# Kernel optimization log

Hardware: AMD Instinct MI355X
Metric: run time of the kernel (lower is better)

Reference implementation:

```python
import jax, jax.numpy as jnp
import numpy as np

LAM = 1e-05
NUM_POINTS = 300
THRESHOLD = 0.5


def _sobel(img):
    # img: [B, 1, H, W] -> edge magnitude [B, 1, H, W]
    kx = jnp.array([[-1., 0., 1.], [-2., 0., 2.], [-1., 0., 1.]], jnp.float32).reshape(1, 1, 3, 3)
    ky = jnp.array([[-1., -2., -1.], [0., 0., 0.], [1., 2., 1.]], jnp.float32).reshape(1, 1, 3, 3)
    dn = jax.lax.conv_dimension_numbers(img.shape, kx.shape, ('NCHW', 'OIHW', 'NCHW'))
    ex = jax.lax.conv_general_dilated(img, kx, (1, 1), ((1, 1), (1, 1)), dimension_numbers=dn)
    ey = jax.lax.conv_general_dilated(img, ky, (1, 1), ((1, 1), (1, 1)), dimension_numbers=dn)
    return jnp.sqrt(ex ** 2 + ey ** 2)


def _select_points(edge_map, key):
    # JIT-friendly analogue of nonzero + randperm[:300]: random scores on
    # above-threshold pixels, take top NUM_POINTS; invalid slots are padded
    # with a duplicate of the first valid point (zero-length MST edges, so
    # they contribute nothing to total persistence, matching fewer points).
    H, W = edge_map.shape
    flat = edge_map.reshape(-1)
    mask = flat > THRESHOLD
    scores = jnp.where(mask, jax.random.uniform(key, flat.shape), -jnp.inf)
    _, idx = jax.lax.top_k(scores, NUM_POINTS)
    valid = mask[idx]
    pts = jnp.stack([idx // W, idx % W], axis=-1).astype(jnp.float32)  # (row, col)
    pts = jnp.where(valid[:, None], pts, pts[0])
    return pts


def _mst_total_persistence(pts):
    # H0 persistence of a Vietoris-Rips complex: births are 0, deaths are the
    # MST edge lengths (Prim's algorithm via lax.scan over N-1 steps).
    # total_persistence with exponent q=2: sum(death^2).
    d2 = jnp.sum((pts[:, None, :] - pts[None, :, :]) ** 2, axis=-1)
    D = jnp.sqrt(jnp.maximum(d2, 0.0))  # [N, N]
    n = pts.shape[0]
    in_tree = jnp.zeros((n,), dtype=bool).at[0].set(True)

    def step(carry, _):
        in_tree, mind = carry
        m = jnp.where(in_tree, jnp.inf, mind)
        j = jnp.argmin(m)
        w = m[j]
        in_tree = in_tree.at[j].set(True)
        mind = jnp.minimum(mind, D[j])
        return (in_tree, mind), w

    _, deaths = jax.lax.scan(step, (in_tree, D[0]), None, length=n - 1)
    return jnp.sum(deaths ** 2)


def _topo_loss(model_output, labels):
    pred_edges = _sobel(jax.nn.sigmoid(model_output))[:, 0]  # [B, H, W]
    mask_edges = _sobel(labels)[:, 0]                         # [B, H, W]
    B = pred_edges.shape[0]
    keys = jax.random.split(jax.random.key(42), 2 * B).reshape(B, 2)

    def per_sample(pe, me, k):
        pts_p = _select_points(pe, k[0])
        pts_m = _select_points(me, k[1])
        tp_p = _mst_total_persistence(pts_p)
        tp_m = _mst_total_persistence(pts_m)
        # SummaryStatisticLoss(total_persistence): |stat(mask) - stat(pred)|
        return jnp.abs(tp_m - tp_p)

    losses = jax.vmap(per_sample)(pred_edges, mask_edges, keys)
    return LAM * jnp.sum(losses) / B


def setup_inputs() -> dict:
    key = jax.random.key(0)
    k1, k2 = jax.random.split(key)
    model_output = jax.random.normal(k1, (32, 1, 512, 512), dtype=jnp.float32)
    labels = jax.random.uniform(k2, (32, 1, 512, 512), dtype=jnp.float32)
    return {"model_output": model_output, "labels": labels}


def reference(model_output, labels):
    return _topo_loss(model_output, labels)
```

## Files before the change

### kernel.cpp

```cpp
#include <hip/hip_runtime.h>
#include <cstdint>
#include <cstddef>

#define NPIX (512 * 512)
#define NMAPS 64
#define NPTS 300
#define CAP 1024
#define LCAP 640
#define NWORDS 4096
#define TARGET 700.0
#define MT_FIXED 8368608u

__device__ __forceinline__ uint32_t umin32(uint32_t a, uint32_t b) {
  return a < b ? a : b;
}

__device__ __forceinline__ void tf2x32(uint32_t k0, uint32_t k1,
                                       uint32_t x0, uint32_t x1,
                                       uint32_t& o0, uint32_t& o1) {
  uint32_t ks2 = k0 ^ k1 ^ 0x1BD11BDAu;
#define TFR(r) { x0 += x1; x1 = (x1 << (r)) | (x1 >> (32 - (r))); x1 ^= x0; }
  x0 += k0; x1 += k1;
  TFR(13) TFR(15) TFR(26) TFR(6)
  x0 += k1; x1 += ks2 + 1u;
  TFR(17) TFR(29) TFR(16) TFR(24)
  x0 += ks2; x1 += k0 + 2u;
  TFR(13) TFR(15) TFR(26) TFR(6)
  x0 += k0; x1 += k1 + 3u;
  TFR(17) TFR(29) TFR(16) TFR(24)
  x0 += k1; x1 += ks2 + 4u;
  TFR(13) TFR(15) TFR(26) TFR(6)
  x0 += ks2; x1 += k0 + 5u;
#undef TFR
  o0 = x0; o1 = x1;
}

__device__ __forceinline__ uint32_t score23(uint32_t k0, uint32_t k1, uint32_t p) {
  uint32_t a, b;
  tf2x32(k0, k1, 0u, p, a, b);
  return (a ^ b) >> 9;
}

__device__ __forceinline__ void map_key(int m, uint32_t& k0, uint32_t& k1) {
  tf2x32(0u, 42u, 0u, (uint32_t)m, k0, k1);
}

template <int CTRL>
__device__ __forceinline__ uint32_t dpp_mov_u32(uint32_t x) {
  return (uint32_t)__builtin_amdgcn_update_dpp((int)x, (int)x, CTRL, 0xF, 0xF,
                                               false);
}

__device__ __forceinline__ uint32_t wave_min_u32_bcast(uint32_t v) {
  v = umin32(v, dpp_mov_u32<0x111>(v));
  v = umin32(v, dpp_mov_u32<0x112>(v));
  v = umin32(v, dpp_mov_u32<0x114>(v));
  v = umin32(v, dpp_mov_u32<0x118>(v));
  v = umin32(v, dpp_mov_u32<0x142>(v));
  v = umin32(v, dpp_mov_u32<0x143>(v));
  return (uint32_t)__builtin_amdgcn_readlane((int)v, 63);
}

__global__ __launch_bounds__(256) void edge_collect_kernel(
    const float* __restrict__ mo, const float* __restrict__ lb,
    unsigned long long* __restrict__ bitmap, unsigned int* __restrict__ wcnts,
    unsigned long long* __restrict__ cand, unsigned int* __restrict__ gcnt32,
    float* __restrict__ out) {
  const int m = blockIdx.y;
  const int which = m & 1;
  const float* __restrict__ src = (which ? lb : mo) + (size_t)(m >> 1) * NPIX;
  const int l = threadIdx.x & 63;
  const int wi = blockIdx.x * 4 + (threadIdx.x >> 6);
  const int cs = wi & 7;
  const int seg = wi >> 3;
  const int y0 = seg * 32;
  const int X = cs * 64 + l;
  const int hcol = (l == 0) ? X - 1 : ((l == 63) ? X + 1 : -1);

  if (m == 0 && blockIdx.x == 0 && threadIdx.x == 0) out[0] = 0.f;

  __shared__ unsigned long long lbuf[LCAP];
  __shared__ unsigned int lcnt;
  __shared__ unsigned int lbase;
  if (threadIdx.x == 0) lcnt = 0;
  __syncthreads();

  uint32_t k0, k1;
  map_key(m, k0, k1);

  auto sig = [&](float t) {
    return which ? t : 1.f / (1.f + __expf(-t));
  };
  auto ldmain = [&](int row) -> float {
    return ((unsigned)row < 512u) ? sig(src[row * 512 + X]) : 0.f;
  };
  auto ldhalo = [&](int row) -> float {
    return ((unsigned)row < 512u && (unsigned)hcol < 512u)
               ? sig(src[row * 512 + hcol]) : 0.f;
  };

  float a = ldmain(y0 - 1), ha = ldhalo(y0 - 1);
  float b = ldmain(y0),     hb = ldhalo(y0);
  unsigned int cnt = 0;

  for (int i = 0; i < 32; ++i) {
    const int y = y0 + i;
    float c = ldmain(y + 1), hc = ldhalo(y + 1);

    float aL = __shfl_up(a, 1);   if (l == 0)  aL = ha;
    float aR = __shfl_down(a, 1); if (l == 63) aR = ha;
    float bL = __shfl_up(b, 1);   if (l == 0)  bL = hb;
    float bR = __shfl_down(b, 1); if (l == 63) bR = hb;
    float cL = __shfl_up(c, 1);   if (l == 0)  cL = hc;
    float cR = __shfl_down(c, 1); if (l == 63) cR = hc;

    float ex = (aR - aL) + 2.f * (bR - bL) + (cR - cL);
    float ey = (cL + 2.f * c + cR) - (aL + 2.f * a + aR);
    bool bit = (ex * ex + ey * ey) > 0.25f;

    unsigned long long ball = __ballot(bit);
    if (l == 0) {
      bitmap[(size_t)m * NWORDS + (size_t)y * 8 + cs] = ball;
      cnt += (unsigned int)__popcll(ball);
    }
    if (bit) {
      uint32_t p = (uint32_t)(y * 512 + X);
      uint32_t sc = score23(k0, k1, p);
      if (sc >= MT_FIXED) {
        unsigned int pos = atomicAdd(&lcnt, 1u);
        if (pos < LCAP)
          lbuf[pos] = ((unsigned long long)sc << 32) | (uint32_t)(~p);
      }
    }
    a = b; ha = hb; b = c; hb = hc;
  }
  if (l == 0) wcnts[m * 128 + wi] = cnt;

  __syncthreads();
  unsigned int cc = lcnt < LCAP ? lcnt : LCAP;
  if (threadIdx.x == 0)
    lbase = atomicAdd(&gcnt32[m * 32], lcnt + (lcnt > LCAP ? 0x1000000u : 0u));
  __syncthreads();
  for (unsigned int i = threadIdx.x; i < cc; i += 256) {
    unsigned int pos = lbase + i;
    if (pos < CAP) cand[(size_t)m * CAP + pos] = lbuf[i];
  }
}

__device__ __forceinline__ void reduce_N(const unsigned int* __restrict__ wcnts,
                                         int m, int tid, unsigned int* sN) {
  if (tid < 64) {
    unsigned int v = wcnts[m * 128 + tid] + wcnts[m * 128 + 64 + tid];
#pragma unroll
    for (int off = 32; off > 0; off >>= 1) v += __shfl_xor(v, off, 64);
    if (tid == 0) *sN = v;
  }
}

__global__ __launch_bounds__(256) void select_kernel(
    const unsigned long long* __restrict__ bitmap,
    const unsigned int* __restrict__ wcnts,
    const unsigned long long* __restrict__ cand,
    const unsigned int* __restrict__ gcnt32,
    uint32_t* __restrict__ pts, unsigned int* __restrict__ nsel) {
  const int m = blockIdx.x;
  const int tid = threadIdx.x;
  __shared__ unsigned long long buf[CAP];
  __shared__ unsigned int hist[256];
  __shared__ unsigned int s_tot, s_cnt, s_b, s_rank, sN;

  reduce_N(wcnts, m, tid, &sN);
  __syncthreads();
  const unsigned int N = sN;
  if (N == 0) { if (tid == 0) nsel[m] = 0; return; }
  const unsigned int need = N < NPTS ? N : NPTS;

  unsigned int c;
  const unsigned int g = gcnt32[m * 32];
  if (g >= need && g <= CAP) {
    c = g;
    for (unsigned int i = tid; i < c; i += 256)
      buf[i] = cand[(size_t)m * CAP + i];
    __syncthreads();
  } else {
    uint32_t k0, k1;
    map_key(m, k0, k1);
    const unsigned long long* __restrict__ wmap = bitmap + (size_t)m * NWORDS;
    unsigned int mt = 0, cnt = 0;
    double target = TARGET;
    for (int iter = 0; iter < 16; ++iter) {
      mt = ((double)N > target)
               ? (unsigned int)(8388608.0 * (1.0 - target / (double)N))
               : 0u;
      if (tid == 0) s_tot = 0;
      __syncthreads();
      unsigned int lc = 0;
      for (int w = tid; w < NWORDS; w += 256) {
        unsigned long long word = wmap[w];
        while (word) {
          int bpos = __builtin_ctzll(word);
          word &= word - 1;
          uint32_t p = ((uint32_t)w << 6) + (uint32_t)bpos;
          lc += (score23(k0, k1, p) >= mt) ? 1u : 0u;
        }
      }
      if (lc) atomicAdd(&s_tot, lc);
      __syncthreads();
      cnt = s_tot;
      __syncthreads();
      if (cnt >= need && cnt <= CAP) break;
      if (cnt < need) target *= 3.0; else target *= 0.5;
    }
    if (tid == 0) s_cnt = 0;
    __syncthreads();
    for (int w = tid; w < NWORDS; w += 256) {
      unsigned long long word = wmap[w];
      while (word) {
        int bpos = __builtin_ctzll(word);
        word &= word - 1;
        uint32_t p = ((uint32_t)w << 6) + (uint32_t)bpos;
        uint32_t sc = score23(k0, k1, p);
        if (sc >= mt) {
          unsigned int pos = atomicAdd(&s_cnt, 1u);
          if (pos < CAP)
            buf[pos] = ((unsigned long long)sc << 32) | (uint32_t)(~p);
        }
      }
    }
    __syncthreads();
    c = s_cnt < CAP ? s_cnt : CAP;
    __syncthreads();
  }

  unsigned long long T = 0ull;
  if (c > need) {
    unsigned int rank = need;
    unsigned long long prefix = 0ull;
    for (int sh = 48; sh >= 0; sh -= 8) {
      hist[tid] = 0;
      __syncthreads();
      for (unsigned int i = tid; i < c; i += 256) {
        unsigned long long k = buf[i];
        if ((k >> (sh + 8)) == (prefix >> (sh + 8)))
          atomicAdd(&hist[(unsigned int)(k >> sh) & 255u], 1u);
      }
      __syncthreads();
      if (tid < 64) {
        unsigned int h0 = hist[4 * tid], h1 = hist[4 * tid + 1];
        unsigned int h2 = hist[4 * tid + 2], h3 = hist[4 * tid + 3];
        unsigned int gsum = h0 + h1 + h2 + h3;
        unsigned int s = gsum;
#pragma unroll
        for (int off = 1; off < 64; off <<= 1) {
          unsigned int o = __shfl_down(s, off, 64);
          s += (tid + off < 64) ? o : 0u;
        }
        unsigned int above = s - gsum;
        unsigned int S3 = above, S2 = S3 + h3, S1 = S2 + h2, S0 = S1 + h1;
        if (S3 < rank && rank <= S3 + h3) { s_b = 4 * tid + 3; s_rank = rank - S3; }
        if (S2 < rank && rank <= S2 + h2) { s_b = 4 * tid + 2; s_rank = rank - S2; }
        if (S1 < rank && rank <= S1 + h1) { s_b = 4 * tid + 1; s_rank = rank - S1; }
        if (S0 < rank && rank <= S0 + h0) { s_b = 4 * tid + 0; s_rank = rank - S0; }
      }
      __syncthreads();
      prefix |= ((unsigned long long)s_b) << sh;
      rank = s_rank;
    }
    T = prefix;
  }

  if (tid == 0) s_cnt = 0;
  __syncthreads();
  for (unsigned int i = tid; i < c; i += 256) {
    unsigned long long k = buf[i];
    if (k >= T) {
      unsigned int pos = atomicAdd(&s_cnt, 1u);
      if (pos < NPTS) {
        uint32_t p = ~(uint32_t)k;
        pts[(size_t)m * NPTS + pos] = ((p >> 9) << 16) | (p & 511u);
      }
    }
  }
  __syncthreads();
  if (tid == 0) nsel[m] = s_cnt < need ? s_cnt : need;
}

__global__ __launch_bounds__(128, 1) void mst_kernel(
    const uint32_t* __restrict__ pts, const unsigned int* __restrict__ nsel,
    float* __restrict__ out) {
  const int wv = threadIdx.x >> 6;
  const int m = blockIdx.x * 2 + wv;
  const int l = threadIdx.x & 63;
  const int n = (int)nsel[m];
  __shared__ float stp[2];

  unsigned int utp = 0;
  if (n > 1) {
    uint32_t pk[5], key[5];
    int px[5], py[5];
#pragma unroll
    for (int k = 0; k < 5; ++k) {
      int id = k * 64 + l;
      pk[k] = (id < n) ? pts[(size_t)m * NPTS + id] : 0u;
    }
    const uint32_t p0 = (uint32_t)__builtin_amdgcn_readlane((int)pk[0], 0);
    const int x0 = (int)(p0 >> 16), y0 = (int)(p0 & 0xFFFFu);
#pragma unroll
    for (int k = 0; k < 5; ++k) {
      int id = k * 64 + l;
      px[k] = (int)(pk[k] >> 16);
      py[k] = (int)(pk[k] & 0xFFFFu);
      if (id > 0 && id < n) {
        int dx = px[k] - x0, dy = py[k] - y0;
        key[k] = ((uint32_t)(__mul24(dx, dx) + __mul24(dy, dy)) << 9) |
                 (uint32_t)id;
      } else {
        key[k] = 0xFFFFFFFFu;
      }
    }

    for (int it = 0; it < n - 1; ++it) {
      uint32_t best = umin32(umin32(umin32(key[0], key[1]),
                                    umin32(key[2], key[3])), key[4]);
      best = wave_min_u32_bcast(best);
      utp += best >> 9;
      const int j = (int)(best & 511u);
      const int ko = j >> 6, lo = j & 63;
      uint32_t cp = pk[0];
#pragma unroll
      for (int k = 1; k < 5; ++k) cp = (ko == k) ? pk[k] : cp;
      const uint32_t pj = (uint32_t)__builtin_amdgcn_readlane((int)cp, lo);
      const int jx = (int)(pj >> 16), jy = (int)(pj & 0xFFFFu);
#pragma unroll
      for (int k = 0; k < 5; ++k) {
        int dx = px[k] - jx, dy = py[k] - jy;
        uint32_t nk = ((uint32_t)(__mul24(dx, dx) + __mul24(dy, dy)) << 9) |
                      (uint32_t)(k * 64 + l);
        uint32_t upd =
            (key[k] == 0xFFFFFFFFu) ? 0xFFFFFFFFu : umin32(key[k], nk);
        key[k] = (k == ko && l == lo) ? 0xFFFFFFFFu : upd;
      }
    }
  }
  if (l == 0) stp[wv] = (float)utp;
  __syncthreads();
  if (threadIdx.x == 0)
    atomicAdd(out, 1e-5f * fabsf(stp[1] - stp[0]) / 32.f);
}

extern "C" void kernel_launch(void* const* d_in, const int* in_sizes, int n_in,
                              void* d_out, int out_size, void* d_ws,
                              size_t ws_size, hipStream_t stream) {
  const float* mo = (const float*)d_in[0];
  const float* lb = (const float*)d_in[1];
  float* out = (float*)d_out;
  char* ws = (char*)d_ws;

  unsigned long long* bitmap = (unsigned long long*)ws;
  unsigned long long* cand = (unsigned long long*)(ws + 2097152);
  unsigned int* wcnts  = (unsigned int*)(ws + 2621440);
  unsigned int* gcnt32 = (unsigned int*)(ws + 2654208);
  unsigned int* nsel   = (unsigned int*)(ws + 2662400);
  uint32_t* pts        = (uint32_t*)(ws + 2662656);

  hipMemsetAsync(gcnt32, 0, 8192, stream);
  edge_collect_kernel<<<dim3(32, 64), 256, 0, stream>>>(mo, lb, bitmap, wcnts,
                                                        cand, gcnt32, out);
  select_kernel<<<NMAPS, 256, 0, stream>>>(bitmap, wcnts, cand, gcnt32, pts,
                                           nsel);
  mst_kernel<<<32, 128, 0, stream>>>(pts, nsel, out);
}
```

Baseline: 246.8 us.

## Use per-block candidate slots, separable Sobel, and templated bounds checks in edge pass

Candidate collection now gives each block a fixed slot region and its own count, so the global atomic counter and its memset launch are gone. The select kernel compacts these regions using a prefix sum over the block counts. The Sobel stencil is computed separably, which cuts the shuffles per row from six to four. Edge-body variants are templated on sigmoid-versus-identity and on whether the tile touches the image border, so interior tiles skip row bounds checks. The raw threefry bits are compared against a threshold instead of calling score23, and the larger CAP grows the select kernel's shared buffer to 16KB.

```diff
diff --git a/kernel.cpp b/kernel.cpp
--- a/kernel.cpp
+++ b/kernel.cpp
@@ -5,11 +5,12 @@
 #define NPIX (512 * 512)
 #define NMAPS 64
 #define NPTS 300
-#define CAP 1024
-#define LCAP 640
+#define CAP 2048
+#define SLOTS 64
+#define LBUFSZ 256
 #define NWORDS 4096
 #define TARGET 700.0
-#define MT_FIXED 8368608u
+#define MT_BITS 0xFF63C000u
 
 __device__ __forceinline__ uint32_t umin32(uint32_t a, uint32_t b) {
   return a < b ? a : b;
@@ -61,61 +62,55 @@
   return (uint32_t)__builtin_amdgcn_readlane((int)v, 63);
 }
 
-__global__ __launch_bounds__(256) void edge_collect_kernel(
-    const float* __restrict__ mo, const float* __restrict__ lb,
-    unsigned long long* __restrict__ bitmap, unsigned int* __restrict__ wcnts,
-    unsigned long long* __restrict__ cand, unsigned int* __restrict__ gcnt32,
-    float* __restrict__ out) {
-  const int m = blockIdx.y;
-  const int which = m & 1;
-  const float* __restrict__ src = (which ? lb : mo) + (size_t)(m >> 1) * NPIX;
-  const int l = threadIdx.x & 63;
-  const int wi = blockIdx.x * 4 + (threadIdx.x >> 6);
-  const int cs = wi & 7;
-  const int seg = wi >> 3;
+template <bool PRED, bool YIN>
+__device__ __forceinline__ void edge_body(
+    const float* __restrict__ src, unsigned long long* __restrict__ bitmap,
+    unsigned int* __restrict__ wcnts, unsigned long long* lbuf,
+    unsigned int* lcnt, int m, int l, int cs, int seg, int wi, uint32_t k0,
+    uint32_t k1) {
   const int y0 = seg * 32;
   const int X = cs * 64 + l;
   const int hcol = (l == 0) ? X - 1 : ((l == 63) ? X + 1 : -1);
-
-  if (m == 0 && blockIdx.x == 0 && threadIdx.x == 0) out[0] = 0.f;
-
-  __shared__ unsigned long long lbuf[LCAP];
-  __shared__ unsigned int lcnt;
-  __shared__ unsigned int lbase;
-  if (threadIdx.x == 0) lcnt = 0;
-  __syncthreads();
-
-  uint32_t k0, k1;
-  map_key(m, k0, k1);
-
-  auto sig = [&](float t) {
-    return which ? t : 1.f / (1.f + __expf(-t));
+  const bool hok = (unsigned)hcol < 512u;
+
+  auto val = [&](float t) -> float {
+    if constexpr (PRED) return 1.f / (1.f + __expf(-t));
+    else return t;
   };
-  auto ldmain = [&](int row) -> float {
-    return ((unsigned)row < 512u) ? sig(src[row * 512 + X]) : 0.f;
+  auto ldm = [&](int row) -> float {
+    if constexpr (!YIN) {
+      if ((unsigned)row >= 512u) return 0.f;
+    }
+    return val(src[row * 512 + X]);
   };
-  auto ldhalo = [&](int row) -> float {
-    return ((unsigned)row < 512u && (unsigned)hcol < 512u)
-               ? sig(src[row * 512 + hcol]) : 0.f;
+  auto ldh = [&](int row) -> float {
+    if (!hok) return 0.f;
+    if constexpr (!YIN) {
+      if ((unsigned)row >= 512u) return 0.f;
+    }
+    return val(src[row * 512 + hcol]);
   };
 
-  float a = ldmain(y0 - 1), ha = ldhalo(y0 - 1);
-  float b = ldmain(y0),     hb = ldhalo(y0);
+  float a = ldm(y0 - 1), b = ldm(y0);
+  float ha = ldh(y0 - 1), hb = ldh(y0);
   unsigned int cnt = 0;
 
   for (int i = 0; i < 32; ++i) {
     const int y = y0 + i;
-    float c = ldmain(y + 1), hc = ldhalo(y + 1);
-
-    float aL = __shfl_up(a, 1);   if (l == 0)  aL = ha;
-    float aR = __shfl_down(a, 1); if (l == 63) aR = ha;
-    float bL = __shfl_up(b, 1);   if (l == 0)  bL = hb;
-    float bR = __shfl_down(b, 1); if (l == 63) bR = hb;
-    float cL = __shfl_up(c, 1);   if (l == 0)  cL = hc;
-    float cR = __shfl_down(c, 1); if (l == 63) cR = hc;
-
-    float ex = (aR - aL) + 2.f * (bR - bL) + (cR - cL);
-    float ey = (cL + 2.f * c + cR) - (aL + 2.f * a + aR);
+    float c = ldm(y + 1), hc = ldh(y + 1);
+
+    float t = a + 2.f * b + c;
+    float u = c - a;
+    float th = ha + 2.f * hb + hc;
+    float uh = hc - ha;
+
+    float tL = __shfl_up(t, 1);   if (l == 0)  tL = th;
+    float tR = __shfl_down(t, 1); if (l == 63) tR = th;
+    float uL = __shfl_up(u, 1);   if (l == 0)  uL = uh;
+    float uR = __shfl_down(u, 1); if (l == 63) uR = uh;
+
+    float ex = tR - tL;
+    float ey = uL + 2.f * u + uR;
     bool bit = (ex * ex + ey * ey) > 0.25f;
 
     unsigned long long ball = __ballot(bit);
@@ -125,26 +120,59 @@
     }
     if (bit) {
       uint32_t p = (uint32_t)(y * 512 + X);
-      uint32_t sc = score23(k0, k1, p);
-      if (sc >= MT_FIXED) {
-        unsigned int pos = atomicAdd(&lcnt, 1u);
-        if (pos < LCAP)
-          lbuf[pos] = ((unsigned long long)sc << 32) | (uint32_t)(~p);
-      }
-    }
-    a = b; ha = hb; b = c; hb = hc;
+      uint32_t o0, o1;
+      tf2x32(k0, k1, 0u, p, o0, o1);
+      uint32_t x = o0 ^ o1;
+      if (x >= MT_BITS) {
+        unsigned int pos = atomicAdd(lcnt, 1u);
+        if (pos < LBUFSZ)
+          lbuf[pos] = ((unsigned long long)(x >> 9) << 32) | (uint32_t)(~p);
+      }
+    }
+    a = b; b = c; ha = hb; hb = hc;
   }
   if (l == 0) wcnts[m * 128 + wi] = cnt;
-
-  __syncthreads();
-  unsigned int cc = lcnt < LCAP ? lcnt : LCAP;
-  if (threadIdx.x == 0)
-    lbase = atomicAdd(&gcnt32[m * 32], lcnt + (lcnt > LCAP ? 0x1000000u : 0u));
-  __syncthreads();
-  for (unsigned int i = threadIdx.x; i < cc; i += 256) {
-    unsigned int pos = lbase + i;
-    if (pos < CAP) cand[(size_t)m * CAP + pos] = lbuf[i];
-  }
+}
+
+__global__ __launch_bounds__(256) void edge_collect_kernel(
+    const float* __restrict__ mo, const float* __restrict__ lb,
+    unsigned long long* __restrict__ bitmap, unsigned int* __restrict__ wcnts,
+    unsigned long long* __restrict__ cand, unsigned int* __restrict__ bcnt,
+    float* __restrict__ out) {
+  const int m = blockIdx.y;
+  const int which = m & 1;
+  const int bx = blockIdx.x;
+  const float* __restrict__ src = (which ? lb : mo) + (size_t)(m >> 1) * NPIX;
+  const int l = threadIdx.x & 63;
+  const int wi = bx * 4 + (threadIdx.x >> 6);
+  const int cs = wi & 7;
+  const int seg = wi >> 3;
+
+  if (m == 0 && bx == 0 && threadIdx.x == 0) out[0] = 0.f;
+
+  __shared__ unsigned long long lbuf[LBUFSZ];
+  __shared__ unsigned int lcnt;
+  if (threadIdx.x == 0) lcnt = 0;
+  __syncthreads();
+
+  uint32_t k0, k1;
+  map_key(m, k0, k1);
+
+  const bool yin = (seg != 0) && (seg != 15);
+  if (which) {
+    if (yin) edge_body<false, true>(src, bitmap, wcnts, lbuf, &lcnt, m, l, cs, seg, wi, k0, k1);
+    else     edge_body<false, false>(src, bitmap, wcnts, lbuf, &lcnt, m, l, cs, seg, wi, k0, k1);
+  } else {
+    if (yin) edge_body<true, true>(src, bitmap, wcnts, lbuf, &lcnt, m, l, cs, seg, wi, k0, k1);
+    else     edge_body<true, false>(src, bitmap, wcnts, lbuf, &lcnt, m, l, cs, seg, wi, k0, k1);
+  }
+
+  __syncthreads();
+  const unsigned int total = lcnt;
+  const unsigned int cc = total < SLOTS ? total : SLOTS;
+  for (unsigned int i = threadIdx.x; i < cc; i += 256)
+    cand[(size_t)m * CAP + bx * SLOTS + i] = lbuf[i];
+  if (threadIdx.x == 0) bcnt[m * 32 + bx] = total;
 }
 
 __device__ __forceinline__ void reduce_N(const unsigned int* __restrict__ wcnts,
@@ -161,26 +189,43 @@
     const unsigned long long* __restrict__ bitmap,
     const unsigned int* __restrict__ wcnts,
     const unsigned long long* __restrict__ cand,
-    const unsigned int* __restrict__ gcnt32,
+    const unsigned int* __restrict__ bcnt,
     uint32_t* __restrict__ pts, unsigned int* __restrict__ nsel) {
   const int m = blockIdx.x;
   const int tid = threadIdx.x;
   __shared__ unsigned long long buf[CAP];
   __shared__ unsigned int hist[256];
-  __shared__ unsigned int s_tot, s_cnt, s_b, s_rank, sN;
+  __shared__ unsigned int scnt32[32];
+  __shared__ unsigned int sbase[33];
+  __shared__ unsigned int s_tot, s_cnt, s_b, s_rank, sN, s_ovf;
 
   reduce_N(wcnts, m, tid, &sN);
+  if (tid < 32) scnt32[tid] = bcnt[m * 32 + tid];
   __syncthreads();
   const unsigned int N = sN;
   if (N == 0) { if (tid == 0) nsel[m] = 0; return; }
   const unsigned int need = N < NPTS ? N : NPTS;
 
+  if (tid == 0) {
+    unsigned int s = 0, ovf = 0;
+    for (int i = 0; i < 32; ++i) {
+      sbase[i] = s;
+      unsigned int cg = scnt32[i];
+      if (cg > SLOTS) ovf = 1;
+      s += cg < SLOTS ? cg : SLOTS;
+    }
+    sbase[32] = s;
+    s_ovf = ovf;
+  }
+  __syncthreads();
+
   unsigned int c;
-  const unsigned int g = gcnt32[m * 32];
-  if (g >= need && g <= CAP) {
-    c = g;
-    for (unsigned int i = tid; i < c; i += 256)
-      buf[i] = cand[(size_t)m * CAP + i];
+  if (!s_ovf && sbase[32] >= need) {
+    c = sbase[32];
+    const int g = tid >> 3, j0 = tid & 7;
+    const unsigned int cg = scnt32[g] < SLOTS ? scnt32[g] : SLOTS;
+    for (unsigned int i = j0; i < cg; i += 8)
+      buf[sbase[g] + i] = cand[(size_t)m * CAP + g * SLOTS + i];
     __syncthreads();
   } else {
     uint32_t k0, k1;
@@ -358,15 +403,14 @@
 
   unsigned long long* bitmap = (unsigned long long*)ws;
   unsigned long long* cand = (unsigned long long*)(ws + 2097152);
-  unsigned int* wcnts  = (unsigned int*)(ws + 2621440);
-  unsigned int* gcnt32 = (unsigned int*)(ws + 2654208);
-  unsigned int* nsel   = (unsigned int*)(ws + 2662400);
-  uint32_t* pts        = (uint32_t*)(ws + 2662656);
-
-  hipMemsetAsync(gcnt32, 0, 8192, stream);
+  unsigned int* wcnts = (unsigned int*)(ws + 3145728);
+  unsigned int* bcnt  = (unsigned int*)(ws + 3178496);
+  unsigned int* nsel  = (unsigned int*)(ws + 3186688);
+  uint32_t* pts       = (uint32_t*)(ws + 3186944);
+
   edge_collect_kernel<<<dim3(32, 64), 256, 0, stream>>>(mo, lb, bitmap, wcnts,
-                                                        cand, gcnt32, out);
-  select_kernel<<<NMAPS, 256, 0, stream>>>(bitmap, wcnts, cand, gcnt32, pts,
+                                                        cand, bcnt, out);
+  select_kernel<<<NMAPS, 256, 0, stream>>>(bitmap, wcnts, cand, bcnt, pts,
                                            nsel);
   mst_kernel<<<32, 128, 0, stream>>>(pts, nsel, out);
 }
```

New measurement: 238.7 us. 3.3% less time.
